# Performance work log

Measured on AMD Instinct MI355X. Metric: run time of the kernel, lower is better.

## Reference

```python
import jax, jax.numpy as jnp
import numpy as np

N_NODES = 100000
N_EDGES = 1600000
D_IN = 64
D_HID = 64
D_OUT = 64


def sage_conv(x, src, dst, W_l, W_r, b, n_nodes):
    # PyG SAGEConv (aggr='mean'): out = lin_l(mean_{j in N(i)} x_j) + lin_r(x_i)
    msg = x[src]                                   # [E, d] gather (irregular)
    agg = jax.ops.segment_sum(msg, dst, num_segments=n_nodes)   # [N, d]
    cnt = jax.ops.segment_sum(jnp.ones((src.shape[0], 1), x.dtype), dst,
                              num_segments=n_nodes)             # [N, 1]
    mean = agg / jnp.maximum(cnt, 1.0)
    return mean @ W_l + x @ W_r + b


def setup_inputs() -> dict:
    key = jax.random.key(0)
    k_x, k_e, k1, k2, k3, k4 = jax.random.split(key, 6)
    x = jax.random.normal(k_x, (N_NODES, D_IN), dtype=jnp.float32)
    edge_index = jax.random.randint(k_e, (2, N_EDGES), 0, N_NODES, dtype=jnp.int64)
    s = 1.0 / np.sqrt(D_IN)
    W_l1 = jax.random.uniform(k1, (D_IN, D_HID), jnp.float32, -s, s)
    W_r1 = jax.random.uniform(k2, (D_IN, D_HID), jnp.float32, -s, s)
    b1 = jnp.zeros((D_HID,), jnp.float32)
    s2 = 1.0 / np.sqrt(D_HID)
    W_l2 = jax.random.uniform(k3, (D_HID, D_OUT), jnp.float32, -s2, s2)
    W_r2 = jax.random.uniform(k4, (D_HID, D_OUT), jnp.float32, -s2, s2)
    b2 = jnp.zeros((D_OUT,), jnp.float32)
    return {"x": x, "edge_index": edge_index,
            "W_l1": W_l1, "W_r1": W_r1, "b1": b1,
            "W_l2": W_l2, "W_r2": W_r2, "b2": b2}


def reference(x, edge_index, W_l1, W_r1, b1, W_l2, W_r2, b2):
    src, dst = edge_index[0], edge_index[1]
    n = x.shape[0]
    h = sage_conv(x, src, dst, W_l1, W_r1, b1, n)
    h = jax.nn.relu(h)
    # dropout is identity in eval mode (training=False)
    out = sage_conv(h, src, dst, W_l2, W_r2, b2, n)
    return out
```

## Files before the change

### kernel.cpp

```cpp
#include <hip/hip_runtime.h>

#define DFEAT 64
#define SBSH 10
#define SBN 1024
#define NSB 98
#define ETILE 4096
#define PACKSH 17
#define SRCMASK 0x1FFFF
#define MSTRIDE 68

typedef __bf16 bf16x8 __attribute__((ext_vector_type(8)));
typedef float f32x4 __attribute__((ext_vector_type(4)));

__device__ __forceinline__ unsigned bf16_rne(float v) {
    unsigned bits = __float_as_uint(v);
    return (bits + 0x7FFFu + ((bits >> 16) & 1u)) >> 16;
}
__device__ __forceinline__ float lo16(unsigned u) { return __uint_as_float(u << 16); }
__device__ __forceinline__ float hi16(unsigned u) { return __uint_as_float(u & 0xFFFF0000u); }

__global__ __launch_bounds__(512) void setup_kernel(
    const int* __restrict__ dst, int n_edges, int nt, int* __restrict__ counts,
    const float* __restrict__ x, unsigned short* __restrict__ xb, int ncvt,
    const float* __restrict__ Wl1, const float* __restrict__ Wr1,
    const float* __restrict__ Wl2, const float* __restrict__ Wr2,
    unsigned short* __restrict__ wpack) {
    int b = blockIdx.x, t = threadIdx.x;
    if (b < nt) {
        __shared__ int lh[NSB];
        if (t < NSB) lh[t] = 0;
        __syncthreads();
        int s0 = b * ETILE;
        int s1 = s0 + ETILE; if (s1 > n_edges) s1 = n_edges;
        for (int e = s0 + t; e < s1; e += 512)
            atomicAdd(&lh[dst[e] >> SBSH], 1);
        __syncthreads();
        if (t < NSB) counts[t * nt + b] = lh[t];
    } else if (b < nt + 4) {
        int u = (b - nt) * 512 + t;
        int l = u & 63;
        int ct = (u >> 6) & 3;
        int chunk = (u >> 8) & 1;
        int gemm = (u >> 9) & 1;
        int layer = (u >> 10) & 1;
        const float* W = layer ? (gemm ? Wr2 : Wl2) : (gemm ? Wr1 : Wl1);
        int col = ct * 16 + (l & 15);
        int k0 = chunk * 32 + (l >> 4) * 8;
        unsigned hi[8], lo[8];
#pragma unroll
        for (int j = 0; j < 8; ++j) {
            float w = W[(k0 + j) * DFEAT + col];
            unsigned h = bf16_rne(w);
            float whi = __uint_as_float(h << 16);
            lo[j] = bf16_rne(w - whi);
            hi[j] = h;
        }
        size_t fh = ((((size_t)(layer * 2 + gemm) * 2 + 0) * 2 + chunk) * 4 + ct) * 64 + l;
        size_t fl = ((((size_t)(layer * 2 + gemm) * 2 + 1) * 2 + chunk) * 4 + ct) * 64 + l;
        int4 vh, vl;
        vh.x = hi[0] | (hi[1] << 16); vh.y = hi[2] | (hi[3] << 16);
        vh.z = hi[4] | (hi[5] << 16); vh.w = hi[6] | (hi[7] << 16);
        vl.x = lo[0] | (lo[1] << 16); vl.y = lo[2] | (lo[3] << 16);
        vl.z = lo[4] | (lo[5] << 16); vl.w = lo[6] | (lo[7] << 16);
        ((int4*)wpack)[fh] = vh;
        ((int4*)wpack)[fl] = vl;
    } else {
        int i = (b - nt - 4) * 512 + t;
        if (i < ncvt) {
            const float4* xp = (const float4*)x;
            float4 a = xp[2 * i], c = xp[2 * i + 1];
            int4 o;
            o.x = bf16_rne(a.x) | (bf16_rne(a.y) << 16);
            o.y = bf16_rne(a.z) | (bf16_rne(a.w) << 16);
            o.z = bf16_rne(c.x) | (bf16_rne(c.y) << 16);
            o.w = bf16_rne(c.z) | (bf16_rne(c.w) << 16);
            ((int4*)xb)[i] = o;
        }
    }
}

__global__ __launch_bounds__(512) void tscan1_kernel(const int* __restrict__ counts,
                                                     int nt,
                                                     int* __restrict__ tilebase,
                                                     int* __restrict__ sbtot) {
    __shared__ int sdata[512];
    int sb = blockIdx.x, t = threadIdx.x;
    int v = (t < nt) ? counts[sb * nt + t] : 0;
    sdata[t] = v;
    __syncthreads();
    for (int off = 1; off < 512; off <<= 1) {
        int x = (t >= off) ? sdata[t - off] : 0;
        __syncthreads();
        sdata[t] += x;
        __syncthreads();
    }
    if (t < nt) tilebase[sb * nt + t] = sdata[t] - v;
    if (t == 511) sbtot[sb] = sdata[511];
}

__global__ __launch_bounds__(128) void tscan2_kernel(const int* __restrict__ sbtot,
                                                     int* __restrict__ sbbase,
                                                     int n_edges) {
    __shared__ int sdata[128];
    int t = threadIdx.x;
    int v = (t < NSB) ? sbtot[t] : 0;
    sdata[t] = v;
    __syncthreads();
    for (int off = 1; off < 128; off <<= 1) {
        int x = (t >= off) ? sdata[t - off] : 0;
        __syncthreads();
        sdata[t] += x;
        __syncthreads();
    }
    if (t < NSB) sbbase[t] = sdata[t] - v;
    if (t == 0) sbbase[NSB] = n_edges;
}

__global__ __launch_bounds__(512) void partition_kernel(const int* __restrict__ src,
                                                        const int* __restrict__ dst,
                                                        int n_edges, int nt,
                                                        const int* __restrict__ tilebase,
                                                        const int* __restrict__ sbbase,
                                                        int* __restrict__ tmp) {
    __shared__ int lcur[NSB];
    int t = threadIdx.x;
    if (t < NSB) lcur[t] = sbbase[t] + tilebase[t * nt + blockIdx.x];
    __syncthreads();
    int s0 = blockIdx.x * ETILE;
    int s1 = s0 + ETILE; if (s1 > n_edges) s1 = n_edges;
    for (int e = s0 + t; e < s1; e += 512) {
        int d = dst[e];
        int sb = d >> SBSH;
        int ofs = atomicAdd(&lcur[sb], 1);
        tmp[ofs] = ((d & (SBN - 1)) << PACKSH) | src[e];
    }
}

__global__ __launch_bounds__(1024) void bucket_sort_kernel(
    const int* __restrict__ sbbase, const int* __restrict__ tmp,
    int* __restrict__ col_src, int* __restrict__ row_ptr,
    int n_nodes, int n_edges) {
    __shared__ int cnt[SBN];
    __shared__ int scan[SBN];
    int b = blockIdx.x, t = threadIdx.x;
    int gb = sbbase[b], ge = sbbase[b + 1];
    cnt[t] = 0;
    __syncthreads();
    for (int e = gb + t; e < ge; e += 1024)
        atomicAdd(&cnt[((unsigned)tmp[e]) >> PACKSH], 1);
    __syncthreads();
    int v = cnt[t];
    scan[t] = v;
    __syncthreads();
    for (int off = 1; off < 1024; off <<= 1) {
        int x = (t >= off) ? scan[t - off] : 0;
        __syncthreads();
        scan[t] += x;
        __syncthreads();
    }
    int excl = scan[t] - v;
    int node = (b << SBSH) + t;
    if (node < n_nodes) row_ptr[node] = gb + excl;
    cnt[t] = gb + excl;
    if (b == (int)gridDim.x - 1 && t == 0) row_ptr[n_nodes] = n_edges;
    __syncthreads();
    for (int e = gb + t; e < ge; e += 1024) {
        int pk = tmp[e];
        int pos = atomicAdd(&cnt[((unsigned)pk) >> PACKSH], 1);
        col_src[pos] = (pk & SRCMASK) << 7;
    }
}

__device__ __forceinline__ void gather16(const int* __restrict__ col_src,
                                         const char* __restrict__ xb8,
                                         int base, int end, int lane, int g4,
                                         float acc[4]) {
    for (; base < end; base += 64) {
        int m = end - base; if (m > 64) m = 64;
        int soff = col_src[base + (lane < m ? lane : 0)];
        for (int i = 0; i < m; i += 16) {
#pragma unroll
            for (int k = 0; k < 4; ++k) {
                int s4 = i + 4 * k;
                if (s4 < m) {
                    int n = s4 + g4;
                    int off = __shfl(soff, n < m ? n : 0);
                    float f = (n < m) ? 1.f : 0.f;
                    int2 v = *(const int2*)(xb8 + off);
                    acc[0] += f * lo16((unsigned)v.x);
                    acc[1] += f * hi16((unsigned)v.x);
                    acc[2] += f * lo16((unsigned)v.y);
                    acc[3] += f * hi16((unsigned)v.y);
                }
            }
        }
    }
}

template <bool RELU, bool OUT_BF16>
__global__ __launch_bounds__(512, 8) void sage_kernel(
    const int* __restrict__ row_ptr, const int* __restrict__ col_src,
    const unsigned short* __restrict__ xb,
    const unsigned short* __restrict__ wpk,
    const float* __restrict__ bias, void* __restrict__ outp, int n_nodes) {
    __shared__ unsigned short sMean[16 * MSTRIDE];
    int t = threadIdx.x;
    int w = t >> 6;
    int lane = t & 63;
    int g4 = lane >> 4;
    int p4 = lane & 15;
    int node0 = blockIdx.x * 16;
    const char* xb8 = (const char*)xb + p4 * 8;

    int nA = node0 + w;
    int nB = node0 + w + 8;
    int ncA = nA < n_nodes ? nA : n_nodes - 1;
    int ncB = nB < n_nodes ? nB : n_nodes - 1;
    int baseA = row_ptr[ncA], endA = row_ptr[ncA + 1];
    int baseB = row_ptr[ncB], endB = row_ptr[ncB + 1];
    int degA = endA - baseA, degB = endB - baseB;

    float accA[4] = {0.f, 0.f, 0.f, 0.f};
    float accB[4] = {0.f, 0.f, 0.f, 0.f};
    gather16(col_src, xb8, baseA, endA, lane, g4, accA);
    gather16(col_src, xb8, baseB, endB, lane, g4, accB);

#pragma unroll
    for (int e = 0; e < 4; ++e) {
        accA[e] += __shfl_xor(accA[e], 16); accA[e] += __shfl_xor(accA[e], 32);
        accB[e] += __shfl_xor(accB[e], 16); accB[e] += __shfl_xor(accB[e], 32);
    }

    if (g4 == 0) {
        float invA = degA > 0 ? 1.f / (float)degA : 0.f;
        float invB = degB > 0 ? 1.f / (float)degB : 0.f;
        int2 oA, oB;
        oA.x = bf16_rne(accA[0] * invA) | (bf16_rne(accA[1] * invA) << 16);
        oA.y = bf16_rne(accA[2] * invA) | (bf16_rne(accA[3] * invA) << 16);
        oB.x = bf16_rne(accB[0] * invB) | (bf16_rne(accB[1] * invB) << 16);
        oB.y = bf16_rne(accB[2] * invB) | (bf16_rne(accB[3] * invB) << 16);
        *(int2*)&sMean[w * MSTRIDE + p4 * 4] = oA;
        *(int2*)&sMean[(w + 8) * MSTRIDE + p4 * 4] = oB;
    }
    __syncthreads();

    if (w < 4) {
        int ct = w;
        int row16 = lane & 15;
        int kq = lane >> 4;
        bf16x8 aA0 = *(const bf16x8*)&sMean[row16 * MSTRIDE + kq * 8];
        bf16x8 aA1 = *(const bf16x8*)&sMean[row16 * MSTRIDE + 32 + kq * 8];
        int xr = node0 + row16; if (xr >= n_nodes) xr = n_nodes - 1;
        const char* xp = (const char*)xb + (size_t)xr * 128 + kq * 16;
        bf16x8 aX0 = *(const bf16x8*)xp;
        bf16x8 aX1 = *(const bf16x8*)(xp + 64);

        const bf16x8* wp = (const bf16x8*)wpk;
        float bcol = bias[ct * 16 + row16];
        f32x4 acc = {bcol, bcol, bcol, bcol};
        acc = __builtin_amdgcn_mfma_f32_16x16x32_bf16(aA0, wp[0 * 256 + ct * 64 + lane], acc, 0, 0, 0);
        acc = __builtin_amdgcn_mfma_f32_16x16x32_bf16(aA1, wp[1 * 256 + ct * 64 + lane], acc, 0, 0, 0);
        acc = __builtin_amdgcn_mfma_f32_16x16x32_bf16(aA0, wp[2 * 256 + ct * 64 + lane], acc, 0, 0, 0);
        acc = __builtin_amdgcn_mfma_f32_16x16x32_bf16(aA1, wp[3 * 256 + ct * 64 + lane], acc, 0, 0, 0);
        acc = __builtin_amdgcn_mfma_f32_16x16x32_bf16(aX0, wp[4 * 256 + ct * 64 + lane], acc, 0, 0, 0);
        acc = __builtin_amdgcn_mfma_f32_16x16x32_bf16(aX1, wp[5 * 256 + ct * 64 + lane], acc, 0, 0, 0);
        acc = __builtin_amdgcn_mfma_f32_16x16x32_bf16(aX0, wp[6 * 256 + ct * 64 + lane], acc, 0, 0, 0);
        acc = __builtin_amdgcn_mfma_f32_16x16x32_bf16(aX1, wp[7 * 256 + ct * 64 + lane], acc, 0, 0, 0);
#pragma unroll
        for (int reg = 0; reg < 4; ++reg) {
            int row = kq * 4 + reg;
            int gn = node0 + row;
            if (gn < n_nodes) {
                float v = acc[reg];
                if (RELU) v = fmaxf(v, 0.0f);
                if (OUT_BF16) {
                    ((unsigned short*)outp)[(size_t)gn * DFEAT + ct * 16 + row16] =
                        (unsigned short)bf16_rne(v);
                } else {
                    ((float*)outp)[(size_t)gn * DFEAT + ct * 16 + row16] = v;
                }
            }
        }
    }
}

extern "C" void kernel_launch(void* const* d_in, const int* in_sizes, int n_in,
                              void* d_out, int out_size, void* d_ws, size_t ws_size,
                              hipStream_t stream) {
    const float* x   = (const float*)d_in[0];
    const int*   ei  = (const int*)d_in[1];
    const float* Wl1 = (const float*)d_in[2];
    const float* Wr1 = (const float*)d_in[3];
    const float* b1  = (const float*)d_in[4];
    const float* Wl2 = (const float*)d_in[5];
    const float* Wr2 = (const float*)d_in[6];
    const float* b2  = (const float*)d_in[7];
    float* out = (float*)d_out;

    int n_nodes = in_sizes[0] / DFEAT;
    int n_edges = in_sizes[1] / 2;
    const int* src  = ei;
    const int* dstv = ei + n_edges;
    int nt = (n_edges + ETILE - 1) / ETILE;

    auto align = [](size_t v) { return (v + 255) & ~(size_t)255; };
    char* ws = (char*)d_ws;
    int* counts   = (int*)ws;            ws += align((size_t)NSB * nt * 4);
    int* tilebase = (int*)ws;            ws += align((size_t)NSB * nt * 4);
    int* sbtot    = (int*)ws;            ws += align(NSB * 4);
    int* sbbase   = (int*)ws;            ws += align((NSB + 1) * 4);
    int* row_ptr  = (int*)ws;            ws += align(((size_t)n_nodes + 1) * 4);
    int* col_src  = (int*)ws;            ws += align((size_t)n_edges * 4);
    unsigned short* xb    = (unsigned short*)ws; ws += align((size_t)n_nodes * DFEAT * 2);
    unsigned short* hb    = (unsigned short*)ws; ws += align((size_t)n_nodes * DFEAT * 2);
    unsigned short* wpack = (unsigned short*)ws; ws += align((size_t)32768);
    int* tmp      = (int*)d_out;

    int ncvt = n_nodes * DFEAT / 8;
    int cvtb = (ncvt + 511) / 512;
    setup_kernel<<<nt + 4 + cvtb, 512, 0, stream>>>(dstv, n_edges, nt, counts,
                                                    x, xb, ncvt,
                                                    Wl1, Wr1, Wl2, Wr2, wpack);
    tscan1_kernel<<<NSB, 512, 0, stream>>>(counts, nt, tilebase, sbtot);
    tscan2_kernel<<<1, 128, 0, stream>>>(sbtot, sbbase, n_edges);
    partition_kernel<<<nt, 512, 0, stream>>>(src, dstv, n_edges, nt, tilebase,
                                             sbbase, tmp);
    bucket_sort_kernel<<<NSB, 1024, 0, stream>>>(sbbase, tmp, col_src, row_ptr,
                                                 n_nodes, n_edges);

    int tiles = (n_nodes + 15) / 16;
    sage_kernel<true, true><<<tiles, 512, 0, stream>>>(row_ptr, col_src, xb,
                                                       wpack, b1, hb, n_nodes);
    sage_kernel<false, false><<<tiles, 512, 0, stream>>>(row_ptr, col_src, hb,
                                                         wpack + 2048 * 8, b2,
                                                         out, n_nodes);
}
```

Before: 155.2 us.

## Process 32 nodes per block with four interleaved neighbor gathers per wave

Each block now handles 32 nodes instead of 16, and each wave gathers neighbors for four nodes at once in a single interleaved loop instead of two sequential gathers. This raises memory-level parallelism, with more independent loads in flight per wave, and lets all eight waves do MFMA work instead of only four. The cost is more registers, since there are now 16 accumulators per lane, which may hurt occupancy. It also adds lockstep divergence when the four nodes have very different degrees.

```diff
diff --git a/kernel.cpp b/kernel.cpp
--- a/kernel.cpp
+++ b/kernel.cpp
@@ -171,85 +171,104 @@
     }
 }
 
-__device__ __forceinline__ void gather16(const int* __restrict__ col_src,
-                                         const char* __restrict__ xb8,
-                                         int base, int end, int lane, int g4,
-                                         float acc[4]) {
-    for (; base < end; base += 64) {
-        int m = end - base; if (m > 64) m = 64;
-        int soff = col_src[base + (lane < m ? lane : 0)];
-        for (int i = 0; i < m; i += 16) {
-#pragma unroll
-            for (int k = 0; k < 4; ++k) {
-                int s4 = i + 4 * k;
-                if (s4 < m) {
-                    int n = s4 + g4;
-                    int off = __shfl(soff, n < m ? n : 0);
-                    float f = (n < m) ? 1.f : 0.f;
-                    int2 v = *(const int2*)(xb8 + off);
-                    acc[0] += f * lo16((unsigned)v.x);
-                    acc[1] += f * hi16((unsigned)v.x);
-                    acc[2] += f * lo16((unsigned)v.y);
-                    acc[3] += f * hi16((unsigned)v.y);
-                }
-            }
-        }
-    }
-}
-
 template <bool RELU, bool OUT_BF16>
 __global__ __launch_bounds__(512, 8) void sage_kernel(
     const int* __restrict__ row_ptr, const int* __restrict__ col_src,
     const unsigned short* __restrict__ xb,
     const unsigned short* __restrict__ wpk,
     const float* __restrict__ bias, void* __restrict__ outp, int n_nodes) {
-    __shared__ unsigned short sMean[16 * MSTRIDE];
+    __shared__ unsigned short sMean[32 * MSTRIDE];
     int t = threadIdx.x;
     int w = t >> 6;
     int lane = t & 63;
     int g4 = lane >> 4;
     int p4 = lane & 15;
-    int node0 = blockIdx.x * 16;
+    int tile32 = blockIdx.x * 32;
     const char* xb8 = (const char*)xb + p4 * 8;
 
-    int nA = node0 + w;
-    int nB = node0 + w + 8;
-    int ncA = nA < n_nodes ? nA : n_nodes - 1;
-    int ncB = nB < n_nodes ? nB : n_nodes - 1;
-    int baseA = row_ptr[ncA], endA = row_ptr[ncA + 1];
-    int baseB = row_ptr[ncB], endB = row_ptr[ncB + 1];
-    int degA = endA - baseA, degB = endB - baseB;
-
-    float accA[4] = {0.f, 0.f, 0.f, 0.f};
-    float accB[4] = {0.f, 0.f, 0.f, 0.f};
-    gather16(col_src, xb8, baseA, endA, lane, g4, accA);
-    gather16(col_src, xb8, baseB, endB, lane, g4, accB);
-
-#pragma unroll
-    for (int e = 0; e < 4; ++e) {
-        accA[e] += __shfl_xor(accA[e], 16); accA[e] += __shfl_xor(accA[e], 32);
-        accB[e] += __shfl_xor(accB[e], 16); accB[e] += __shfl_xor(accB[e], 32);
+    int bs[4], en[4], dg[4];
+#pragma unroll
+    for (int j = 0; j < 4; ++j) {
+        int row = ((j & 1) ? w + 8 : w) + ((j & 2) ? 16 : 0);
+        int n = tile32 + row;
+        int nc = n < n_nodes ? n : n_nodes - 1;
+        bs[j] = row_ptr[nc];
+        en[j] = row_ptr[nc + 1];
+        dg[j] = en[j] - bs[j];
+    }
+
+    float acc[4][4] = {{0.f}};
+    bool more = true;
+    while (more) {
+        int m[4], soff[4];
+#pragma unroll
+        for (int j = 0; j < 4; ++j) {
+            int mm = en[j] - bs[j];
+            mm = mm > 64 ? 64 : mm;
+            m[j] = mm;
+            soff[j] = (mm > 0) ? col_src[bs[j] + (lane < mm ? lane : 0)] : 0;
+        }
+        int mmax = m[0];
+#pragma unroll
+        for (int j = 1; j < 4; ++j) mmax = m[j] > mmax ? m[j] : mmax;
+        for (int i = 0; i < mmax; i += 16) {
+#pragma unroll
+            for (int k = 0; k < 4; ++k) {
+                int s4 = i + 4 * k;
+                int n = s4 + g4;
+#pragma unroll
+                for (int j = 0; j < 4; ++j) {
+                    if (s4 < m[j]) {
+                        int off = __shfl(soff[j], n < m[j] ? n : 0);
+                        float f = (n < m[j]) ? 1.f : 0.f;
+                        int2 v = *(const int2*)(xb8 + off);
+                        acc[j][0] += f * lo16((unsigned)v.x);
+                        acc[j][1] += f * hi16((unsigned)v.x);
+                        acc[j][2] += f * lo16((unsigned)v.y);
+                        acc[j][3] += f * hi16((unsigned)v.y);
+                    }
+                }
+            }
+        }
+        more = false;
+#pragma unroll
+        for (int j = 0; j < 4; ++j) {
+            bs[j] += 64;
+            more = more || (bs[j] < en[j]);
+        }
+    }
+
+#pragma unroll
+    for (int j = 0; j < 4; ++j) {
+#pragma unroll
+        for (int e = 0; e < 4; ++e) {
+            acc[j][e] += __shfl_xor(acc[j][e], 16);
+            acc[j][e] += __shfl_xor(acc[j][e], 32);
+        }
     }
 
     if (g4 == 0) {
-        float invA = degA > 0 ? 1.f / (float)degA : 0.f;
-        float invB = degB > 0 ? 1.f / (float)degB : 0.f;
-        int2 oA, oB;
-        oA.x = bf16_rne(accA[0] * invA) | (bf16_rne(accA[1] * invA) << 16);
-        oA.y = bf16_rne(accA[2] * invA) | (bf16_rne(accA[3] * invA) << 16);
-        oB.x = bf16_rne(accB[0] * invB) | (bf16_rne(accB[1] * invB) << 16);
-        oB.y = bf16_rne(accB[2] * invB) | (bf16_rne(accB[3] * invB) << 16);
-        *(int2*)&sMean[w * MSTRIDE + p4 * 4] = oA;
-        *(int2*)&sMean[(w + 8) * MSTRIDE + p4 * 4] = oB;
-    }
-    __syncthreads();
-
-    if (w < 4) {
-        int ct = w;
+#pragma unroll
+        for (int j = 0; j < 4; ++j) {
+            float inv = dg[j] > 0 ? 1.f / (float)dg[j] : 0.f;
+            int2 o;
+            o.x = bf16_rne(acc[j][0] * inv) | (bf16_rne(acc[j][1] * inv) << 16);
+            o.y = bf16_rne(acc[j][2] * inv) | (bf16_rne(acc[j][3] * inv) << 16);
+            int row = ((j & 1) ? w + 8 : w) + ((j & 2) ? 16 : 0);
+            *(int2*)&sMean[row * MSTRIDE + p4 * 4] = o;
+        }
+    }
+    __syncthreads();
+
+    {
+        int tile = w >> 2;
+        int ct = w & 3;
         int row16 = lane & 15;
         int kq = lane >> 4;
-        bf16x8 aA0 = *(const bf16x8*)&sMean[row16 * MSTRIDE + kq * 8];
-        bf16x8 aA1 = *(const bf16x8*)&sMean[row16 * MSTRIDE + 32 + kq * 8];
+        int node0 = tile32 + tile * 16;
+        int srow = tile * 16 + row16;
+        bf16x8 aA0 = *(const bf16x8*)&sMean[srow * MSTRIDE + kq * 8];
+        bf16x8 aA1 = *(const bf16x8*)&sMean[srow * MSTRIDE + 32 + kq * 8];
         int xr = node0 + row16; if (xr >= n_nodes) xr = n_nodes - 1;
         const char* xp = (const char*)xb + (size_t)xr * 128 + kq * 16;
         bf16x8 aX0 = *(const bf16x8*)xp;
@@ -257,21 +276,21 @@
 
         const bf16x8* wp = (const bf16x8*)wpk;
         float bcol = bias[ct * 16 + row16];
-        f32x4 acc = {bcol, bcol, bcol, bcol};
-        acc = __builtin_amdgcn_mfma_f32_16x16x32_bf16(aA0, wp[0 * 256 + ct * 64 + lane], acc, 0, 0, 0);
-        acc = __builtin_amdgcn_mfma_f32_16x16x32_bf16(aA1, wp[1 * 256 + ct * 64 + lane], acc, 0, 0, 0);
-        acc = __builtin_amdgcn_mfma_f32_16x16x32_bf16(aA0, wp[2 * 256 + ct * 64 + lane], acc, 0, 0, 0);
-        acc = __builtin_amdgcn_mfma_f32_16x16x32_bf16(aA1, wp[3 * 256 + ct * 64 + lane], acc, 0, 0, 0);
-        acc = __builtin_amdgcn_mfma_f32_16x16x32_bf16(aX0, wp[4 * 256 + ct * 64 + lane], acc, 0, 0, 0);
-        acc = __builtin_amdgcn_mfma_f32_16x16x32_bf16(aX1, wp[5 * 256 + ct * 64 + lane], acc, 0, 0, 0);
-        acc = __builtin_amdgcn_mfma_f32_16x16x32_bf16(aX0, wp[6 * 256 + ct * 64 + lane], acc, 0, 0, 0);
-        acc = __builtin_amdgcn_mfma_f32_16x16x32_bf16(aX1, wp[7 * 256 + ct * 64 + lane], acc, 0, 0, 0);
+        f32x4 acc2 = {bcol, bcol, bcol, bcol};
+        acc2 = __builtin_amdgcn_mfma_f32_16x16x32_bf16(aA0, wp[0 * 256 + ct * 64 + lane], acc2, 0, 0, 0);
+        acc2 = __builtin_amdgcn_mfma_f32_16x16x32_bf16(aA1, wp[1 * 256 + ct * 64 + lane], acc2, 0, 0, 0);
+        acc2 = __builtin_amdgcn_mfma_f32_16x16x32_bf16(aA0, wp[2 * 256 + ct * 64 + lane], acc2, 0, 0, 0);
+        acc2 = __builtin_amdgcn_mfma_f32_16x16x32_bf16(aA1, wp[3 * 256 + ct * 64 + lane], acc2, 0, 0, 0);
+        acc2 = __builtin_amdgcn_mfma_f32_16x16x32_bf16(aX0, wp[4 * 256 + ct * 64 + lane], acc2, 0, 0, 0);
+        acc2 = __builtin_amdgcn_mfma_f32_16x16x32_bf16(aX1, wp[5 * 256 + ct * 64 + lane], acc2, 0, 0, 0);
+        acc2 = __builtin_amdgcn_mfma_f32_16x16x32_bf16(aX0, wp[6 * 256 + ct * 64 + lane], acc2, 0, 0, 0);
+        acc2 = __builtin_amdgcn_mfma_f32_16x16x32_bf16(aX1, wp[7 * 256 + ct * 64 + lane], acc2, 0, 0, 0);
 #pragma unroll
         for (int reg = 0; reg < 4; ++reg) {
             int row = kq * 4 + reg;
             int gn = node0 + row;
             if (gn < n_nodes) {
-                float v = acc[reg];
+                float v = acc2[reg];
                 if (RELU) v = fmaxf(v, 0.0f);
                 if (OUT_BF16) {
                     ((unsigned short*)outp)[(size_t)gn * DFEAT + ct * 16 + row16] =
@@ -328,7 +347,7 @@
     bucket_sort_kernel<<<NSB, 1024, 0, stream>>>(sbbase, tmp, col_src, row_ptr,
                                                  n_nodes, n_edges);
 
-    int tiles = (n_nodes + 15) / 16;
+    int tiles = (n_nodes + 31) / 32;
     sage_kernel<true, true><<<tiles, 512, 0, stream>>>(row_ptr, col_src, xb,
                                                        wpack, b1, hb, n_nodes);
     sage_kernel<false, false><<<tiles, 512, 0, stream>>>(row_ptr, col_src, hb,
```

New measurement: 159.0 us. +2.5%, slower.
